# Kernel tuning notes

Measured on AMD Instinct MI355X. Metric: run time of the kernel, lower is better.

The kernel has to match this reference:

```python
import jax, jax.numpy as jnp
import numpy as np

D_IN = 1024
D_OUT = 1024
NUM_HEADS = 16
HEAD_DIM = D_OUT // NUM_HEADS


def setup_inputs() -> dict:
    key = jax.random.key(0)
    ks = jax.random.split(key, 6)
    scale = 1.0 / np.sqrt(D_IN)
    x = jax.random.normal(ks[0], (4, 2048, D_IN), dtype=jnp.float32)
    # nn.Linear stores weight as [out, in]; we keep [in, out] for x @ W
    W_query = jax.random.uniform(ks[1], (D_IN, D_OUT), jnp.float32, -scale, scale)
    W_key = jax.random.uniform(ks[2], (D_IN, D_OUT), jnp.float32, -scale, scale)
    W_value = jax.random.uniform(ks[3], (D_IN, D_OUT), jnp.float32, -scale, scale)
    W_out = jax.random.uniform(ks[4], (D_OUT, D_OUT), jnp.float32, -scale, scale)
    b_out = jax.random.uniform(ks[5], (D_OUT,), jnp.float32, -scale, scale)
    return {"x": x, "W_query": W_query, "W_key": W_key, "W_value": W_value,
            "W_out": W_out, "b_out": b_out}


def reference(x, W_query, W_key, W_value, W_out, b_out):
    b, n, _ = x.shape
    # QKV projections -> [b, h, n, d]
    def proj(W):
        return (x @ W).reshape(b, n, NUM_HEADS, HEAD_DIM).transpose(0, 2, 1, 3)
    q = proj(W_query)
    k = proj(W_key)
    v = proj(W_value)
    # scaled scores [b, h, n, n] with causal mask
    scores = jnp.einsum('bhqd,bhkd->bhqk', q, k) / jnp.sqrt(jnp.float32(HEAD_DIM))
    causal = jnp.tril(jnp.ones((n, n), dtype=bool))
    scores = jnp.where(causal, scores, -jnp.inf)
    weights = jax.nn.softmax(scores, axis=-1)  # dropout p=0.0 -> identity
    ctx = jnp.einsum('bhqk,bhkd->bhqd', weights, v)
    ctx = ctx.transpose(0, 2, 1, 3).reshape(b, n, D_OUT)
    return ctx @ W_out + b_out
```

## Files before the change

kernel.cpp:

```cpp
#include <hip/hip_runtime.h>
#include <hip/hip_bf16.h>
#include <math.h>


typedef __bf16  bf16x8  __attribute__((ext_vector_type(8)));
typedef __bf16  bf16x2  __attribute__((ext_vector_type(2)));
typedef float   floatx4 __attribute__((ext_vector_type(4)));
typedef short   shortx4 __attribute__((ext_vector_type(4)));

#if __has_builtin(__builtin_amdgcn_mfma_f32_16x16x16bf16_1k)
#define HAVE_MFMA16 1
#endif

__device__ __forceinline__ unsigned short f2bf(float f) {
    __hip_bfloat16 h = __float2bfloat16(f);
    return *reinterpret_cast<unsigned short*>(&h);
}

__device__ __forceinline__ unsigned int pkbf(float a, float b) {
#if __has_builtin(__builtin_amdgcn_cvt_pk_bf16_f32)
    bf16x2 t = __builtin_amdgcn_cvt_pk_bf16_f32(a, b);
    return __builtin_bit_cast(unsigned int, t);
#else
    return (unsigned int)f2bf(a) | ((unsigned int)f2bf(b) << 16);
#endif
}
__device__ __forceinline__ ushort4 pk4(float a, float b, float c, float d) {
    union { ushort4 u; unsigned int w[2]; } u;
    u.w[0] = pkbf(a, b);
    u.w[1] = pkbf(c, d);
    return u.u;
}

__device__ __forceinline__ void gll16(const unsigned short* g, unsigned short* l) {
    __builtin_amdgcn_global_load_lds(
        (const __attribute__((address_space(1))) unsigned int*)g,
        (__attribute__((address_space(3))) unsigned int*)l, 16, 0, 0);
}

__global__ void prep(const float* __restrict__ x, unsigned short* __restrict__ xb,
                     const float* __restrict__ Wq, const float* __restrict__ Wk,
                     const float* __restrict__ Wv, const float* __restrict__ Wo,
                     unsigned short* __restrict__ WT, unsigned short* __restrict__ WoT) {
    __shared__ float tile[32][33];
    int bid = blockIdx.x, tid = threadIdx.x;
    if (bid < 8192) {
        int i = (bid * 256 + tid) * 4;
        float4 v = *(const float4*)(x + i);
        *(ushort4*)(xb + i) = pk4(v.x, v.y, v.z, v.w);
        return;
    }
    int id = bid - 8192;
    int mat = id >> 10, rem = id & 1023;
    const float* src = (mat == 0) ? Wq : (mat == 1) ? Wk : (mat == 2) ? Wv : Wo;
    unsigned short* dst = (mat < 3) ? WT : WoT;
    int nbase = (mat < 3) ? mat * 1024 : 0;
    int kt = (rem & 31) * 32, nt = (rem >> 5) * 32;
    int tx = tid & 31, ty = tid >> 5;
    for (int j = 0; j < 32; j += 8)
        tile[ty + j][tx] = src[(kt + ty + j) * 1024 + nt + tx];
    __syncthreads();
    for (int j = 0; j < 32; j += 8) {
        int n = nt + ty + j;
        dst[(nbase + n) * 1024 + kt + tx] = f2bf(tile[tx][ty + j]);
    }
}

#define FENCE asm volatile("" ::: "memory")

#define LDA_FRAG(dst, MQ)                                              \
    _Pragma("unroll") for (int ks_ = 0; ks_ < 2; ++ks_)                \
    _Pragma("unroll") for (int i_ = 0; i_ < 4; ++i_) {                 \
        int row_ = wm * 128 + (MQ) * 64 + i_ * 16 + lm;                \
        int pu_ = ((ks_ * 4 + quad) ^ (lm & 7)) * 8;                   \
        dst[ks_][i_] = *(const bf16x8*)&Ac[row_ * 64 + pu_];           \
    }

#define LDB_FRAG(dst, NQ)                                              \
    _Pragma("unroll") for (int ks_ = 0; ks_ < 2; ++ks_)                \
    _Pragma("unroll") for (int j_ = 0; j_ < 2; ++j_) {                 \
        int row_ = wn * 64 + (NQ) * 32 + j_ * 16 + lm;                 \
        int pu_ = ((ks_ * 4 + quad) ^ (lm & 7)) * 8;                   \
        dst[ks_][j_] = *(const bf16x8*)&Bc[row_ * 64 + pu_];           \
    }

#define MMA_Q(afr, bfr, MQ, NQ)                                                            \
    __builtin_amdgcn_s_setprio(1);                                                         \
    if (sw) {                                                                              \
        _Pragma("unroll") for (int i_ = 0; i_ < 4; ++i_)                                   \
        _Pragma("unroll") for (int j_ = 0; j_ < 2; ++j_) {                                 \
            floatx4& c_ = acc[(MQ) * 4 + i_][(NQ) * 2 + j_];                               \
            c_ = __builtin_amdgcn_mfma_f32_16x16x32_bf16(bfr[0][j_], afr[0][i_], c_, 0, 0, 0); \
            c_ = __builtin_amdgcn_mfma_f32_16x16x32_bf16(bfr[1][j_], afr[1][i_], c_, 0, 0, 0); \
        }                                                                                  \
    } else {                                                                               \
        _Pragma("unroll") for (int i_ = 0; i_ < 4; ++i_)                                   \
        _Pragma("unroll") for (int j_ = 0; j_ < 2; ++j_) {                                 \
            floatx4& c_ = acc[(MQ) * 4 + i_][(NQ) * 2 + j_];                               \
            c_ = __builtin_amdgcn_mfma_f32_16x16x32_bf16(afr[0][i_], bfr[0][j_], c_, 0, 0, 0); \
            c_ = __builtin_amdgcn_mfma_f32_16x16x32_bf16(afr[1][i_], bfr[1][j_], c_, 0, 0, 0); \
        }                                                                                  \
    }                                                                                      \
    __builtin_amdgcn_s_setprio(0);

__global__ __launch_bounds__(512, 2) void gemm_qkv(const unsigned short* __restrict__ A,
                                                   const unsigned short* __restrict__ B,
                                                   unsigned short* __restrict__ Qo,
                                                   unsigned short* __restrict__ Ko,
                                                   unsigned short* __restrict__ Vo) {
    __shared__ __align__(16) unsigned short As[2][256 * 64];
    __shared__ __align__(16) unsigned short Bs[2][256 * 64];

    int tid = threadIdx.x;
    int lane = tid & 63, w = tid >> 6;
    int wm = w >> 2, wn = w & 3;
    int lm = lane & 15, quad = lane >> 4;

    int bid = blockIdx.x;
    int swz = (bid & 7) * 48 + (bid >> 3);
    int bm = swz / 12, bn = swz % 12;
    int m0 = bm * 256, n0 = bn * 256;
    bool sw = (n0 < 2048);

    const unsigned short* Ag = A + (size_t)m0 * 1024;
    const unsigned short* Bg = B + (size_t)n0 * 1024;

    auto STAGE = [&](int bufi, int kb) {
#pragma unroll
        for (int p = 0; p < 4; ++p) {
            int id = p * 512 + tid;
            int row = id >> 3;
            int cbs = ((id & 7) ^ (row & 7)) * 8;
            int lofs = (p * 512 + w * 64) * 8;
            gll16(&Ag[row * 1024 + kb + cbs], &As[bufi][lofs]);
            gll16(&Bg[row * 1024 + kb + cbs], &Bs[bufi][lofs]);
        }
    };

    floatx4 acc[8][4] = {};

    STAGE(0, 0);
    STAGE(1, 64);
    asm volatile("s_waitcnt vmcnt(8)" ::: "memory");
    FENCE; __builtin_amdgcn_s_barrier(); FENCE;

#pragma unroll 1
    for (int t = 0; t < 16; ++t) {
        const unsigned short* Ac = As[t & 1];
        const unsigned short* Bc = Bs[t & 1];
        bf16x8 a0[2][4], a1[2][4], b0[2][2], b1[2][2];

        LDA_FRAG(a0, 0);
        LDB_FRAG(b0, 0);
        MMA_Q(a0, b0, 0, 0);
        __builtin_amdgcn_s_barrier();
        LDB_FRAG(b1, 1);
        MMA_Q(a0, b1, 0, 1);
        __builtin_amdgcn_s_barrier();
        LDA_FRAG(a1, 1);
        MMA_Q(a1, b1, 1, 1);
        __builtin_amdgcn_s_barrier();
        MMA_Q(a1, b0, 1, 0);

        FENCE; __builtin_amdgcn_s_barrier(); FENCE;
        if (t + 2 < 16) STAGE(t & 1, (t + 2) * 64);
        if (t + 1 < 16) {
            if (t + 2 < 16) { asm volatile("s_waitcnt vmcnt(8)" ::: "memory"); }
            else            { asm volatile("s_waitcnt vmcnt(0)" ::: "memory"); }
            FENCE; __builtin_amdgcn_s_barrier(); FENCE;
        }
    }

    if (sw) {
        bool isQ = (n0 < 1024);
        unsigned short* dst = isQ ? Qo : Ko;
        float qs = isQ ? 0.1803368801f : 1.0f;
#pragma unroll
        for (int mi = 0; mi < 8; ++mi) {
            int s = m0 + wm * 128 + mi * 16 + lm;
            int bb = s >> 11, sl = s & 2047;
#pragma unroll
            for (int ni = 0; ni < 4; ++ni) {
                int gcol0 = n0 + wn * 64 + ni * 16 + quad * 4;
                int h = (gcol0 & 1023) >> 6, d0 = gcol0 & 63;
                *(ushort4*)&dst[(((size_t)(bb * 16 + h) * 2048) + sl) * 64 + d0] =
                    pk4(acc[mi][ni][0] * qs, acc[mi][ni][1] * qs,
                        acc[mi][ni][2] * qs, acc[mi][ni][3] * qs);
            }
        }
    } else {
#pragma unroll
        for (int mi = 0; mi < 8; ++mi) {
            int grow0 = m0 + wm * 128 + mi * 16 + quad * 4;
            int bb = grow0 >> 11, sl = grow0 & 2047;
#pragma unroll
            for (int ni = 0; ni < 4; ++ni) {
                int gcol = n0 + wn * 64 + ni * 16 + lm;
                int hn = gcol & 1023;
                int h = hn >> 6, d = hn & 63;
                *(ushort4*)&Vo[((size_t)(bb * 16 + h) * 64 + d) * 2048 + sl] =
                    pk4(acc[mi][ni][0], acc[mi][ni][1], acc[mi][ni][2], acc[mi][ni][3]);
            }
        }
    }
}

template <int EPI>
__global__ __launch_bounds__(256) void gemm_bt(const unsigned short* __restrict__ A,
                                               const unsigned short* __restrict__ B,
                                               unsigned short* __restrict__ Qo,
                                               unsigned short* __restrict__ Ko,
                                               unsigned short* __restrict__ Vo,
                                               const float* __restrict__ bias,
                                               float* __restrict__ Out) {
    __shared__ __align__(16) unsigned short As[128 * 64];
    __shared__ __align__(16) unsigned short Bs[128 * 64];

    int tid = threadIdx.x;
    int lane = tid & 63, w = tid >> 6;
    int wm = w >> 1, wn = w & 1;
    int lm = lane & 15, quad = lane >> 4;
    int m0 = blockIdx.x * 128, n0 = blockIdx.y * 128;
    bool sw = (EPI == 1) || (n0 < 2048);

    floatx4 acc[4][4] = {};

    for (int kb = 0; kb < 1024; kb += 64) {
        __syncthreads();
        for (int p = 0; p < 4; ++p) {
            int id = p * 256 + tid;
            int row = id >> 3;
            int cbs = ((id & 7) ^ (row & 7)) * 8;
            int lbase = (p * 256 + w * 64) * 8;
            gll16(&A[(m0 + row) * 1024 + kb + cbs], &As[lbase]);
            gll16(&B[(n0 + row) * 1024 + kb + cbs], &Bs[lbase]);
        }
        __syncthreads();
        bf16x8 af[2][4], bf[2][4];
        for (int ks = 0; ks < 2; ++ks)
            for (int i = 0; i < 4; ++i) {
                int pu = (((ks * 4 + quad) ^ (lm & 7))) * 8;
                af[ks][i] = *(const bf16x8*)&As[(wm * 64 + i * 16 + lm) * 64 + pu];
                bf[ks][i] = *(const bf16x8*)&Bs[(wn * 64 + i * 16 + lm) * 64 + pu];
            }
        if (sw) {
            for (int mi = 0; mi < 4; ++mi)
                for (int ni = 0; ni < 4; ++ni) {
                    acc[mi][ni] = __builtin_amdgcn_mfma_f32_16x16x32_bf16(bf[0][ni], af[0][mi], acc[mi][ni], 0, 0, 0);
                    acc[mi][ni] = __builtin_amdgcn_mfma_f32_16x16x32_bf16(bf[1][ni], af[1][mi], acc[mi][ni], 0, 0, 0);
                }
        } else {
            for (int mi = 0; mi < 4; ++mi)
                for (int ni = 0; ni < 4; ++ni) {
                    acc[mi][ni] = __builtin_amdgcn_mfma_f32_16x16x32_bf16(af[0][mi], bf[0][ni], acc[mi][ni], 0, 0, 0);
                    acc[mi][ni] = __builtin_amdgcn_mfma_f32_16x16x32_bf16(af[1][mi], bf[1][ni], acc[mi][ni], 0, 0, 0);
                }
        }
    }

    if constexpr (EPI == 0) {
        if (sw) {
            bool isQ = (n0 < 1024);
            unsigned short* dst = isQ ? Qo : Ko;
            float qs = isQ ? 0.1803368801f : 1.0f;
            for (int mi = 0; mi < 4; ++mi) {
                int s = m0 + wm * 64 + mi * 16 + lm;
                int bb = s >> 11, sl = s & 2047;
                for (int ni = 0; ni < 4; ++ni) {
                    int gcol0 = n0 + wn * 64 + ni * 16 + quad * 4;
                    int h = (gcol0 & 1023) >> 6, d0 = gcol0 & 63;
                    *(ushort4*)&dst[(((size_t)(bb * 16 + h) * 2048) + sl) * 64 + d0] =
                        pk4(acc[mi][ni][0] * qs, acc[mi][ni][1] * qs,
                            acc[mi][ni][2] * qs, acc[mi][ni][3] * qs);
                }
            }
        } else {
            for (int mi = 0; mi < 4; ++mi) {
                int grow0 = m0 + wm * 64 + mi * 16 + quad * 4;
                int bb = grow0 >> 11, sl = grow0 & 2047;
                for (int ni = 0; ni < 4; ++ni) {
                    int gcol = n0 + wn * 64 + ni * 16 + lm;
                    int hn = gcol & 1023;
                    int h = hn >> 6, d = hn & 63;
                    *(ushort4*)&Vo[((size_t)(bb * 16 + h) * 64 + d) * 2048 + sl] =
                        pk4(acc[mi][ni][0], acc[mi][ni][1], acc[mi][ni][2], acc[mi][ni][3]);
                }
            }
        }
    } else {
        for (int mi = 0; mi < 4; ++mi) {
            int s = m0 + wm * 64 + mi * 16 + lm;
            for (int ni = 0; ni < 4; ++ni) {
                int gcol0 = n0 + wn * 64 + ni * 16 + quad * 4;
                float4 bv = *(const float4*)&bias[gcol0];
                float4 o;
                o.x = acc[mi][ni][0] + bv.x; o.y = acc[mi][ni][1] + bv.y;
                o.z = acc[mi][ni][2] + bv.z; o.w = acc[mi][ni][3] + bv.w;
                *(float4*)&Out[(size_t)s * 1024 + gcol0] = o;
            }
        }
    }
}

__global__ __launch_bounds__(512) void attn(const unsigned short* __restrict__ Q,
                                            const unsigned short* __restrict__ K,
                                            const unsigned short* __restrict__ Vt,
                                            unsigned short* __restrict__ ctx) {
    constexpr int LKS = 72;
    __shared__ __align__(16) unsigned short Ks[2][64 * LKS];
    __shared__ __align__(16) unsigned short Vts[2][64 * LKS];

    int tid = threadIdx.x, lane = tid & 63, w = tid >> 6;
    int lm = lane & 15, quad = lane >> 4;
    int blk = blockIdx.x;
    int bh = blk & 63;
    int qt = 15 - (blk >> 6);
    int trips = 2 * qt + 2;
    int tmax = 2 * qt + (w >> 2);
    const unsigned short* Qg  = Q  + (size_t)bh * 2048 * 64;
    const unsigned short* Kg  = K  + (size_t)bh * 2048 * 64;
    const unsigned short* Vtg = Vt + (size_t)bh * 64 * 2048;

    int qrow = qt * 128 + w * 16 + lm;
    bf16x8 aq0 = *(const bf16x8*)&Qg[qrow * 64 + quad * 8];
    bf16x8 aq1 = *(const bf16x8*)&Qg[qrow * 64 + 32 + quad * 8];

    floatx4 O[4] = {};
    float lrow = 0.f;

    int r0 = tid >> 3, c0 = (tid & 7) * 8;

    {
        uint4 k0 = *(const uint4*)&Kg[r0 * 64 + c0];
        uint4 v0 = *(const uint4*)&Vtg[r0 * 2048 + c0];
        *(uint4*)&Ks[0][r0 * LKS + c0]  = k0;
        *(uint4*)&Vts[0][r0 * LKS + c0] = v0;
    }
    __syncthreads();

    for (int t = 0; t < trips; ++t) {
        int cur = t & 1, nxt = cur ^ 1;
        bool pre = (t + 1 < trips);
        uint4 pk, pv;
        if (pre) {
            int kb2 = (t + 1) * 64;
            pk = *(const uint4*)&Kg[(kb2 + r0) * 64 + c0];
            pv = *(const uint4*)&Vtg[r0 * 2048 + kb2 + c0];
        }

        if (t <= tmax) {
            const unsigned short* Kc = Ks[cur];
            const unsigned short* Vc = Vts[cur];

            floatx4 s[4];
            for (int n = 0; n < 4; ++n) {
                bf16x8 a0 = *(const bf16x8*)&Kc[(n * 16 + lm) * LKS + quad * 8];
                bf16x8 a1 = *(const bf16x8*)&Kc[(n * 16 + lm) * LKS + 32 + quad * 8];
                floatx4 z = {};
                z = __builtin_amdgcn_mfma_f32_16x16x32_bf16(a0, aq0, z, 0, 0, 0);
                z = __builtin_amdgcn_mfma_f32_16x16x32_bf16(a1, aq1, z, 0, 0, 0);
                s[n] = z;
            }

            bool diag = (t == tmax);
            if (diag) {
                int qr = (w & 3) * 16 + lm;
                for (int n = 0; n < 4; ++n)
                    for (int r = 0; r < 4; ++r)
                        if (n * 16 + quad * 4 + r > qr) s[n][r] = -INFINITY;
            }
            float p[4][4], rs = 0.f;
            for (int n = 0; n < 4; ++n)
                for (int r = 0; r < 4; ++r) {
                    p[n][r] = __builtin_amdgcn_exp2f(s[n][r]);
                    rs += p[n][r];
                }
            lrow += rs;

#ifdef HAVE_MFMA16
            shortx4 pb[4];
            for (int n = 0; n < 4; ++n) {
                union { shortx4 s4; unsigned int w2[2]; } u;
                u.w2[0] = pkbf(p[n][0], p[n][1]);
                u.w2[1] = pkbf(p[n][2], p[n][3]);
                pb[n] = u.s4;
            }
            for (int dblk = 0; dblk < 4; ++dblk)
                for (int n = 0; n < 4; ++n) {
                    shortx4 va = *(const shortx4*)&Vc[(dblk * 16 + lm) * LKS + n * 16 + quad * 4];
                    O[dblk] = __builtin_amdgcn_mfma_f32_16x16x16bf16_1k(va, pb[n], O[dblk], 0, 0, 0);
                }
#else
            unsigned int dw[4][2];
            for (int n = 0; n < 4; ++n) {
                dw[n][0] = pkbf(p[n][0], p[n][1]);
                dw[n][1] = pkbf(p[n][2], p[n][3]);
            }
            bool hiTile = (quad >> 1);
            for (int hh = 0; hh < 2; ++hh) {
                unsigned int bp[4];
                for (int j = 0; j < 4; ++j) {
                    int srcLane = lm + (((quad & 1) * 2 + (j >> 1)) << 4);
                    unsigned int lo = __shfl((int)dw[2 * hh][j & 1], srcLane);
                    unsigned int hi = __shfl((int)dw[2 * hh + 1][j & 1], srcLane);
                    bp[j] = hiTile ? hi : lo;
                }
                bf16x8 bfrag = *(bf16x8*)bp;
                for (int dblk = 0; dblk < 4; ++dblk) {
                    bf16x8 av = *(const bf16x8*)&Vc[(dblk * 16 + lm) * LKS + hh * 32 + quad * 8];
                    O[dblk] = __builtin_amdgcn_mfma_f32_16x16x32_bf16(av, bfrag, O[dblk], 0, 0, 0);
                }
            }
#endif
        }

        if (pre) {
            *(uint4*)&Ks[nxt][r0 * LKS + c0]  = pk;
            *(uint4*)&Vts[nxt][r0 * LKS + c0] = pv;
        }
        __syncthreads();
    }

    lrow += __shfl_xor(lrow, 16);
    lrow += __shfl_xor(lrow, 32);

    int b = bh >> 4, h = bh & 15;
    int q = qt * 128 + w * 16 + lm;
    float inv = 1.0f / lrow;
    for (int dblk = 0; dblk < 4; ++dblk) {
        *(ushort4*)&ctx[((size_t)(b * 2048 + q)) * 1024 + h * 64 + dblk * 16 + quad * 4] =
            pk4(O[dblk][0] * inv, O[dblk][1] * inv, O[dblk][2] * inv, O[dblk][3] * inv);
    }
}

extern "C" void kernel_launch(void* const* d_in, const int* in_sizes, int n_in,
                              void* d_out, int out_size, void* d_ws, size_t ws_size,
                              hipStream_t stream) {
    const float* x   = (const float*)d_in[0];
    const float* Wq  = (const float*)d_in[1];
    const float* Wk  = (const float*)d_in[2];
    const float* Wv  = (const float*)d_in[3];
    const float* Wo  = (const float*)d_in[4];
    const float* bo  = (const float*)d_in[5];
    float* out = (float*)d_out;

    char* ws = (char*)d_ws;
    unsigned short* xb  = (unsigned short*)(ws);
    unsigned short* WT  = (unsigned short*)(ws + 16777216);
    unsigned short* WoT = (unsigned short*)(ws + 23068672);
    unsigned short* Qb  = (unsigned short*)(ws + 25165824);
    unsigned short* Kb  = (unsigned short*)(ws + 41943040);
    unsigned short* Vtb = (unsigned short*)(ws + 58720256);
    unsigned short* ctx = xb;

    prep<<<12288, 256, 0, stream>>>(x, xb, Wq, Wk, Wv, Wo, WT, WoT);
    gemm_qkv<<<384, 512, 0, stream>>>(xb, WT, Qb, Kb, Vtb);
    attn<<<1024, 512, 0, stream>>>(Qb, Kb, Vtb, ctx);
    gemm_bt<1><<<dim3(64, 8), 256, 0, stream>>>(ctx, WoT, nullptr, nullptr, nullptr, bo, out);
}
```

Measured before the change: 265.9 us.

## Interleave half-tile global loads with MFMA phases in QKV GEMM pipeline

Restructures the QKV projection GEMM main loop into a manually unrolled two-buffer schedule. Global-to-LDS loads are split into half-tiles and issued between MFMA quadrant phases, with barriers and lgkmcnt waits placed around each phase, instead of staging a whole tile after all compute. The block-to-tile mapping is also changed so each XCD covers a contiguous rectangle of M and N tiles for better L2 reuse. The aim is to overlap memory traffic with matrix math more finely, at the cost of many more barriers and a more fragile schedule.

Result: slower. 369.5 us (+39.0%).

```diff
diff --git a/kernel.cpp b/kernel.cpp
--- a/kernel.cpp
+++ b/kernel.cpp
@@ -66,22 +66,26 @@
     }
 }
 
-#define FENCE asm volatile("" ::: "memory")
-
-#define LDA_FRAG(dst, MQ)                                              \
+#define PH_BAR do { asm volatile("" ::: "memory"); \
+                    __builtin_amdgcn_s_barrier();  \
+                    asm volatile("" ::: "memory"); } while (0)
+#define LGKM0  asm volatile("s_waitcnt lgkmcnt(0)" ::: "memory")
+#define VMC(N) asm volatile("s_waitcnt vmcnt(" #N ")" ::: "memory")
+
+#define LDA_FRAG(SRC, dst, MQ)                                         \
     _Pragma("unroll") for (int ks_ = 0; ks_ < 2; ++ks_)                \
     _Pragma("unroll") for (int i_ = 0; i_ < 4; ++i_) {                 \
         int row_ = wm * 128 + (MQ) * 64 + i_ * 16 + lm;                \
         int pu_ = ((ks_ * 4 + quad) ^ (lm & 7)) * 8;                   \
-        dst[ks_][i_] = *(const bf16x8*)&Ac[row_ * 64 + pu_];           \
-    }
-
-#define LDB_FRAG(dst, NQ)                                              \
+        dst[ks_][i_] = *(const bf16x8*)&SRC[row_ * 64 + pu_];          \
+    }
+
+#define LDB_FRAG(SRC, dst, NQ)                                         \
     _Pragma("unroll") for (int ks_ = 0; ks_ < 2; ++ks_)                \
     _Pragma("unroll") for (int j_ = 0; j_ < 2; ++j_) {                 \
         int row_ = wn * 64 + (NQ) * 32 + j_ * 16 + lm;                 \
         int pu_ = ((ks_ * 4 + quad) ^ (lm & 7)) * 8;                   \
-        dst[ks_][j_] = *(const bf16x8*)&Bc[row_ * 64 + pu_];           \
+        dst[ks_][j_] = *(const bf16x8*)&SRC[row_ * 64 + pu_];          \
     }
 
 #define MMA_Q(afr, bfr, MQ, NQ)                                                            \
@@ -117,58 +121,88 @@
     int lm = lane & 15, quad = lane >> 4;
 
     int bid = blockIdx.x;
-    int swz = (bid & 7) * 48 + (bid >> 3);
-    int bm = swz / 12, bn = swz % 12;
+    int xcd = bid & 7, idx = bid >> 3;
+    int cm = xcd & 3, cn = xcd >> 2;
+    int im = idx & 7, in_ = idx >> 3;
+    int bm = cm * 8 + im, bn = cn * 6 + in_;
     int m0 = bm * 256, n0 = bn * 256;
     bool sw = (n0 < 2048);
 
     const unsigned short* Ag = A + (size_t)m0 * 1024;
     const unsigned short* Bg = B + (size_t)n0 * 1024;
-
-    auto STAGE = [&](int bufi, int kb) {
+    unsigned short* As0 = &As[0][0]; unsigned short* As1 = &As[1][0];
+    unsigned short* Bs0 = &Bs[0][0]; unsigned short* Bs1 = &Bs[1][0];
+
+    auto STG = [&](unsigned short* L, const unsigned short* G, int kb, int half) {
 #pragma unroll
-        for (int p = 0; p < 4; ++p) {
+        for (int p = 0; p < 2; ++p) {
             int id = p * 512 + tid;
-            int row = id >> 3;
+            int row = half * 128 + (id >> 3);
             int cbs = ((id & 7) ^ (row & 7)) * 8;
-            int lofs = (p * 512 + w * 64) * 8;
-            gll16(&Ag[row * 1024 + kb + cbs], &As[bufi][lofs]);
-            gll16(&Bg[row * 1024 + kb + cbs], &Bs[bufi][lofs]);
+            gll16(&G[row * 1024 + kb + cbs],
+                  &L[half * 8192 + (p * 512 + w * 64) * 8]);
         }
     };
 
     floatx4 acc[8][4] = {};
 
-    STAGE(0, 0);
-    STAGE(1, 64);
-    asm volatile("s_waitcnt vmcnt(8)" ::: "memory");
-    FENCE; __builtin_amdgcn_s_barrier(); FENCE;
+    STG(As0, Ag, 0, 0);  STG(As0, Ag, 0, 1);
+    STG(Bs0, Bg, 0, 0);  STG(Bs0, Bg, 0, 1);
+    STG(Bs1, Bg, 64, 0); STG(Bs1, Bg, 64, 1);
+    VMC(4);
+    PH_BAR;
 
 #pragma unroll 1
-    for (int t = 0; t < 16; ++t) {
-        const unsigned short* Ac = As[t & 1];
-        const unsigned short* Bc = Bs[t & 1];
+    for (int i = 0; i < 7; ++i) {
+        int k1 = (2 * i + 1) * 64, k2 = (2 * i + 2) * 64, k3 = (2 * i + 3) * 64;
         bf16x8 a0[2][4], a1[2][4], b0[2][2], b1[2][2];
 
-        LDA_FRAG(a0, 0);
-        LDB_FRAG(b0, 0);
-        MMA_Q(a0, b0, 0, 0);
-        __builtin_amdgcn_s_barrier();
-        LDB_FRAG(b1, 1);
-        MMA_Q(a0, b1, 0, 1);
-        __builtin_amdgcn_s_barrier();
-        LDA_FRAG(a1, 1);
-        MMA_Q(a1, b1, 1, 1);
-        __builtin_amdgcn_s_barrier();
+        LDA_FRAG(As0, a0, 0); LDB_FRAG(Bs0, b0, 0);
+        STG(As1, Ag, k1, 0);
+        PH_BAR; LGKM0; MMA_Q(a0, b0, 0, 0); PH_BAR;
+        LDB_FRAG(Bs0, b1, 1);
+        STG(As1, Ag, k1, 1);
+        PH_BAR; LGKM0; MMA_Q(a0, b1, 0, 1); PH_BAR;
+        LDA_FRAG(As0, a1, 1);
+        STG(Bs0, Bg, k2, 0);
+        PH_BAR; LGKM0; MMA_Q(a1, b1, 1, 1); PH_BAR;
+        STG(Bs0, Bg, k2, 1);
+        PH_BAR; MMA_Q(a1, b0, 1, 0);
+        VMC(4);
+        PH_BAR;
+
+        LDA_FRAG(As1, a0, 0); LDB_FRAG(Bs1, b0, 0);
+        STG(As0, Ag, k2, 0);
+        PH_BAR; LGKM0; MMA_Q(a0, b0, 0, 0); PH_BAR;
+        LDB_FRAG(Bs1, b1, 1);
+        STG(As0, Ag, k2, 1);
+        PH_BAR; LGKM0; MMA_Q(a0, b1, 0, 1); PH_BAR;
+        LDA_FRAG(As1, a1, 1);
+        STG(Bs1, Bg, k3, 0);
+        PH_BAR; LGKM0; MMA_Q(a1, b1, 1, 1); PH_BAR;
+        STG(Bs1, Bg, k3, 1);
+        PH_BAR; MMA_Q(a1, b0, 1, 0);
+        VMC(4);
+        PH_BAR;
+    }
+
+    {
+        bf16x8 a0[2][4], a1[2][4], b0[2][2], b1[2][2];
+        LDA_FRAG(As0, a0, 0); LDB_FRAG(Bs0, b0, 0);
+        STG(As1, Ag, 15 * 64, 0);
+        PH_BAR; LGKM0; MMA_Q(a0, b0, 0, 0); PH_BAR;
+        LDB_FRAG(Bs0, b1, 1);
+        STG(As1, Ag, 15 * 64, 1);
+        PH_BAR; LGKM0; MMA_Q(a0, b1, 0, 1); PH_BAR;
+        LDA_FRAG(As0, a1, 1);
+        PH_BAR; LGKM0; MMA_Q(a1, b1, 1, 1);
         MMA_Q(a1, b0, 1, 0);
-
-        FENCE; __builtin_amdgcn_s_barrier(); FENCE;
-        if (t + 2 < 16) STAGE(t & 1, (t + 2) * 64);
-        if (t + 1 < 16) {
-            if (t + 2 < 16) { asm volatile("s_waitcnt vmcnt(8)" ::: "memory"); }
-            else            { asm volatile("s_waitcnt vmcnt(0)" ::: "memory"); }
-            FENCE; __builtin_amdgcn_s_barrier(); FENCE;
-        }
+        VMC(0);
+        PH_BAR;
+        LDA_FRAG(As1, a0, 0); LDB_FRAG(Bs1, b0, 0);
+        LDB_FRAG(Bs1, b1, 1); LDA_FRAG(As1, a1, 1);
+        MMA_Q(a0, b0, 0, 0); MMA_Q(a0, b1, 0, 1);
+        MMA_Q(a1, b1, 1, 1); MMA_Q(a1, b0, 1, 0);
     }
 
     if (sw) {
```
